# Kernel optimization log

Measured on AMD Instinct MI355X. Metric: run time of the kernel, lower is better.

Reference implementation:

```python
import jax, jax.numpy as jnp
import numpy as np

ALPHA = 0.1
BETA = 0.3
MARGIN = 2.0


def setup_inputs() -> dict:
    key = jax.random.key(0)
    k1, k2 = jax.random.split(key)
    prediction = jax.random.normal(k1, (8, 2048, 512), dtype=jnp.float32)
    target_seg = jax.random.randint(k2, (8, 2048), 0, 16, dtype=jnp.int64)
    return {"prediction": prediction, "target_seg": target_seg}


def _pairwise_sqdist(x):
    # x: [n, L, d] -> squared Euclidean distances [n, L, L] via a GEMM
    sq = jnp.sum(x * x, axis=-1)  # [n, L]
    inner = jnp.einsum('nld,nmd->nlm', x, x)  # [n, L, L]
    d2 = sq[:, :, None] + sq[:, None, :] - 2.0 * inner
    return jnp.maximum(d2, 0.0)


def _safe_sqrt(d2):
    # sqrt with zero (not NaN) gradient at 0, matching torch.cdist behavior
    pos = d2 > 0
    return jnp.where(pos, jnp.sqrt(jnp.where(pos, d2, 1.0)), 0.0)


def reference(prediction, target_seg):
    # y[i,j,k] = 1 if target_seg[i,j] == target_seg[i,k]
    y = (target_seg[:, :, None] == target_seg[:, None, :]).astype(prediction.dtype)
    d2 = _pairwise_sqdist(prediction)
    dist = _safe_sqrt(d2)
    hinge = jnp.maximum(MARGIN - dist, 0.0)
    loss = ALPHA * y * d2 + BETA * (1.0 - y) * hinge * hinge
    return jnp.mean(loss)
```

## Files before the change

### kernel.cpp

```cpp
#include <hip/hip_runtime.h>
#include <math.h>

#define L      2048
#define DDIM   512
#define NBATCH 8
#define BM     128
#define BN     128
#define BK     64
#define NKT    (DDIM / BK)
#define NTILE  (L / BM)
#define NPAIR  (NTILE * (NTILE + 1) / 2)
#define TOTAL_BLOCKS (NBATCH * NPAIR)

#define ALPHA  0.1f
#define BETA   0.3f
#define MARGIN 2.0f

typedef _Float16 f16x8 __attribute__((ext_vector_type(8)));
typedef __attribute__((ext_vector_type(16))) float f32x16;

#define TILE_SH 8192
#define BUFSZ   16384

#define GLOAD_LDS16(g, l) __builtin_amdgcn_global_load_lds(              \
    (const __attribute__((address_space(1))) unsigned int*)(g),          \
    (__attribute__((address_space(3))) unsigned int*)(l), 16, 0, 0)

__global__ __launch_bounds__(256) void conv_kernel(const float* __restrict__ pred,
                                                   _Float16* __restrict__ h,
                                                   float* __restrict__ sq) {
    int w     = threadIdx.x >> 6;
    int lane  = threadIdx.x & 63;
    int batch = blockIdx.x & 7;
    int idx   = blockIdx.x >> 3;
    int row   = batch * L + idx * 4 + w;
    const float* p = pred + (size_t)row * DDIM + lane * 8;
    float4 v0 = *(const float4*)(p);
    float4 v1 = *(const float4*)(p + 4);
    float vals[8] = {v0.x, v0.y, v0.z, v0.w, v1.x, v1.y, v1.z, v1.w};
    f16x8 hv;
    float s = 0.0f;
    #pragma unroll
    for (int i = 0; i < 8; ++i) {
        float x = vals[i];
        s = fmaf(x, x, s);
        hv[i] = (_Float16)x;
    }
    *(f16x8*)(h + (size_t)row * DDIM + lane * 8) = hv;
    #pragma unroll
    for (int off = 32; off > 0; off >>= 1) s += __shfl_down(s, off);
    if (lane == 0) sq[row] = s;
}

__global__ __launch_bounds__(256) void loss_kernel(
        const _Float16* __restrict__ h,
        const int*   __restrict__ seg,
        const float* __restrict__ sq,
        double*      __restrict__ partials) {
    __shared__ _Float16 smem[2 * BUFSZ];
    __shared__ double wred[4];

    int bid = blockIdx.x;
    int n = bid & 7;
    int p = bid >> 3;
    int tj = 0;
    while (true) {
        int rl2 = NTILE - tj;
        if (p < rl2) break;
        p -= rl2;
        ++tj;
    }
    int tk = tj + p;
    int j0 = tj * BM, k0 = tk * BN;

    int t    = threadIdx.x;
    int w    = t >> 6;
    int lane = t & 63;
    int wr   = w >> 1, wc = w & 1;
    int l31  = lane & 31;
    int hsel = lane >> 5;

    const _Float16* baseH = h + (size_t)n * L * DDIM;

    int rl8 = lane >> 3;
    int lc  = (lane & 7) ^ rl8;
    const _Float16* srcA = baseH + (size_t)(j0 + w * 32 + rl8) * DDIM + lc * 8;
    const _Float16* srcB = baseH + (size_t)(k0 + w * 32 + rl8) * DDIM + lc * 8;
    _Float16* dstA = smem + w * 2048;
    _Float16* dstB = smem + TILE_SH + w * 2048;

    #define STAGE(kt, cur)                                                    \
    {                                                                         \
        _Pragma("unroll")                                                     \
        for (int q = 0; q < 4; ++q) {                                         \
            GLOAD_LDS16(srcA + (size_t)(q * 8) * DDIM + (kt) * BK,            \
                        dstA + (cur) * BUFSZ + q * 512);                      \
            GLOAD_LDS16(srcB + (size_t)(q * 8) * DDIM + (kt) * BK,            \
                        dstB + (cur) * BUFSZ + q * 512);                      \
        }                                                                     \
    }

    int s7 = l31 & 7;
    int ra = (wr * 64 + l31) * 64;
    int rb = (wc * 64 + l31) * 64 + TILE_SH;
    int iA0 = ra + (((0 + hsel) ^ s7) << 3);
    int iA1 = ra + (((2 + hsel) ^ s7) << 3);
    int iA2 = ra + (((4 + hsel) ^ s7) << 3);
    int iA3 = ra + (((6 + hsel) ^ s7) << 3);
    int iB0 = rb + (((0 + hsel) ^ s7) << 3);
    int iB1 = rb + (((2 + hsel) ^ s7) << 3);
    int iB2 = rb + (((4 + hsel) ^ s7) << 3);
    int iB3 = rb + (((6 + hsel) ^ s7) << 3);

    f32x16 acc[2][2];
    #pragma unroll
    for (int m = 0; m < 2; ++m)
        #pragma unroll
        for (int nn = 0; nn < 2; ++nn)
            #pragma unroll
            for (int r = 0; r < 16; ++r) acc[m][nn][r] = 0.0f;

    STAGE(0, 0);
    asm volatile("s_waitcnt vmcnt(0)" ::: "memory");
    __builtin_amdgcn_s_barrier();

    #pragma unroll
    for (int kt = 0; kt < NKT; ++kt) {
        const int cur = kt & 1;
        if (kt + 1 < NKT) STAGE(kt + 1, cur ^ 1);

        #pragma unroll
        for (int ks = 0; ks < 4; ++ks) {
            int iA = (ks == 0) ? iA0 : (ks == 1) ? iA1 : (ks == 2) ? iA2 : iA3;
            int iB = (ks == 0) ? iB0 : (ks == 1) ? iB1 : (ks == 2) ? iB2 : iB3;
            f16x8 a0 = *(const f16x8*)&smem[iA + cur * BUFSZ];
            f16x8 a1 = *(const f16x8*)&smem[iA + cur * BUFSZ + 2048];
            f16x8 b0 = *(const f16x8*)&smem[iB + cur * BUFSZ];
            f16x8 b1 = *(const f16x8*)&smem[iB + cur * BUFSZ + 2048];
            acc[0][0] = __builtin_amdgcn_mfma_f32_32x32x16_f16(a0, b0, acc[0][0], 0, 0, 0);
            acc[0][1] = __builtin_amdgcn_mfma_f32_32x32x16_f16(a0, b1, acc[0][1], 0, 0, 0);
            acc[1][0] = __builtin_amdgcn_mfma_f32_32x32x16_f16(a1, b0, acc[1][0], 0, 0, 0);
            acc[1][1] = __builtin_amdgcn_mfma_f32_32x32x16_f16(a1, b1, acc[1][1], 0, 0, 0);
        }

        asm volatile("s_waitcnt vmcnt(0)" ::: "memory");
        __builtin_amdgcn_s_barrier();
    }

    const int*   segb = seg + n * L;
    const float* sqb  = sq + n * L;

    float lsum = 0.0f;
    #pragma unroll
    for (int nn = 0; nn < 2; ++nn) {
        int k = k0 + wc * 64 + nn * 32 + l31;
        float sqk = sqb[k];
        int   sgk = segb[k];
        #pragma unroll
        for (int m = 0; m < 2; ++m)
            #pragma unroll
            for (int r = 0; r < 16; ++r) {
                int j = j0 + wr * 64 + m * 32 + (r & 3) + 8 * (r >> 2) + 4 * hsel;
                float inner = acc[m][nn][r];
                float d2 = fmaxf(sqb[j] + sqk - 2.0f * inner, 0.0f);
                float v;
                if (segb[j] == sgk) {
                    v = ALPHA * d2;
                } else {
                    float dist = sqrtf(d2);
                    float hg = fmaxf(MARGIN - dist, 0.0f);
                    v = BETA * hg * hg;
                }
                lsum += v;
            }
    }

    double wgt = (tj == tk) ? 1.0 : 2.0;
    double dsum = (double)lsum * wgt;
    #pragma unroll
    for (int off = 32; off > 0; off >>= 1)
        dsum += __shfl_down(dsum, off);
    if (lane == 0) wred[w] = dsum;
    __syncthreads();
    if (t == 0) partials[bid] = (wred[0] + wred[1]) + (wred[2] + wred[3]);
}

__global__ __launch_bounds__(256) void reduce_kernel(const double* __restrict__ partials,
                                                     float* __restrict__ out,
                                                     int nPart, double invCount) {
    __shared__ double red[256];
    int t = threadIdx.x;
    double s = 0.0;
    for (int i = t; i < nPart; i += 256) s += partials[i];
    red[t] = s;
    __syncthreads();
    #pragma unroll
    for (int k = 128; k > 0; k >>= 1) {
        if (t < k) red[t] += red[t + k];
        __syncthreads();
    }
    if (t == 0) out[0] = (float)(red[0] * invCount);
}

extern "C" void kernel_launch(void* const* d_in, const int* in_sizes, int n_in,
                              void* d_out, int out_size, void* d_ws, size_t ws_size,
                              hipStream_t stream) {
    const float* pred = (const float*)d_in[0];
    const int*   seg  = (const int*)d_in[1];
    float* out = (float*)d_out;

    const size_t HALF = (size_t)NBATCH * L * DDIM;
    _Float16* h        = (_Float16*)d_ws;
    float*    sq       = (float*)(h + HALF);
    double*   partials = (double*)(sq + NBATCH * L);

    conv_kernel<<<NBATCH * L / 4, 256, 0, stream>>>(pred, h, sq);
    loss_kernel<<<TOTAL_BLOCKS, 256, 0, stream>>>(h, seg, sq, partials);
    reduce_kernel<<<1, 256, 0, stream>>>(partials, out, TOTAL_BLOCKS,
                                         1.0 / (double)((size_t)NBATCH * L * L));
}
```

Measured before the change: 62.59 us.

## Replace double-buffered K pipeline with single-buffered 128-wide K stages

```diff
diff --git a/kernel.cpp b/kernel.cpp
--- a/kernel.cpp
+++ b/kernel.cpp
@@ -6,8 +6,8 @@
 #define NBATCH 8
 #define BM     128
 #define BN     128
-#define BK     64
-#define NKT    (DDIM / BK)
+#define BK     128
+#define NST    (DDIM / BK)
 #define NTILE  (L / BM)
 #define NPAIR  (NTILE * (NTILE + 1) / 2)
 #define TOTAL_BLOCKS (NBATCH * NPAIR)
@@ -19,8 +19,8 @@
 typedef _Float16 f16x8 __attribute__((ext_vector_type(8)));
 typedef __attribute__((ext_vector_type(16))) float f32x16;
 
-#define TILE_SH 8192
-#define BUFSZ   16384
+#define AHALF  8192
+#define BOFF   16384
 
 #define GLOAD_LDS16(g, l) __builtin_amdgcn_global_load_lds(              \
     (const __attribute__((address_space(1))) unsigned int*)(g),          \
@@ -57,7 +57,7 @@
         const int*   __restrict__ seg,
         const float* __restrict__ sq,
         double*      __restrict__ partials) {
-    __shared__ _Float16 smem[2 * BUFSZ];
+    __shared__ _Float16 smem[32768];
     __shared__ double wred[4];
 
     int bid = blockIdx.x;
@@ -87,22 +87,24 @@
     const _Float16* srcA = baseH + (size_t)(j0 + w * 32 + rl8) * DDIM + lc * 8;
     const _Float16* srcB = baseH + (size_t)(k0 + w * 32 + rl8) * DDIM + lc * 8;
     _Float16* dstA = smem + w * 2048;
-    _Float16* dstB = smem + TILE_SH + w * 2048;
-
-    #define STAGE(kt, cur)                                                    \
+    _Float16* dstB = smem + BOFF + w * 2048;
+
+    #define STAGE(st)                                                         \
     {                                                                         \
         _Pragma("unroll")                                                     \
-        for (int q = 0; q < 4; ++q) {                                         \
-            GLOAD_LDS16(srcA + (size_t)(q * 8) * DDIM + (kt) * BK,            \
-                        dstA + (cur) * BUFSZ + q * 512);                      \
-            GLOAD_LDS16(srcB + (size_t)(q * 8) * DDIM + (kt) * BK,            \
-                        dstB + (cur) * BUFSZ + q * 512);                      \
-        }                                                                     \
+        for (int q = 0; q < 4; ++q)                                           \
+            _Pragma("unroll")                                                 \
+            for (int kh = 0; kh < 2; ++kh) {                                  \
+                GLOAD_LDS16(srcA + (size_t)(q * 8) * DDIM + (st) * BK + kh * 64, \
+                            dstA + kh * AHALF + q * 512);                     \
+                GLOAD_LDS16(srcB + (size_t)(q * 8) * DDIM + (st) * BK + kh * 64, \
+                            dstB + kh * AHALF + q * 512);                     \
+            }                                                                 \
     }
 
     int s7 = l31 & 7;
     int ra = (wr * 64 + l31) * 64;
-    int rb = (wc * 64 + l31) * 64 + TILE_SH;
+    int rb = (wc * 64 + l31) * 64 + BOFF;
     int iA0 = ra + (((0 + hsel) ^ s7) << 3);
     int iA1 = ra + (((2 + hsel) ^ s7) << 3);
     int iA2 = ra + (((4 + hsel) ^ s7) << 3);
@@ -120,31 +122,29 @@
             #pragma unroll
             for (int r = 0; r < 16; ++r) acc[m][nn][r] = 0.0f;
 
-    STAGE(0, 0);
-    asm volatile("s_waitcnt vmcnt(0)" ::: "memory");
-    __builtin_amdgcn_s_barrier();
-
-    #pragma unroll
-    for (int kt = 0; kt < NKT; ++kt) {
-        const int cur = kt & 1;
-        if (kt + 1 < NKT) STAGE(kt + 1, cur ^ 1);
+    #pragma unroll
+    for (int st = 0; st < NST; ++st) {
+        __syncthreads();
+        STAGE(st);
+        __syncthreads();
 
         #pragma unroll
-        for (int ks = 0; ks < 4; ++ks) {
-            int iA = (ks == 0) ? iA0 : (ks == 1) ? iA1 : (ks == 2) ? iA2 : iA3;
-            int iB = (ks == 0) ? iB0 : (ks == 1) ? iB1 : (ks == 2) ? iB2 : iB3;
-            f16x8 a0 = *(const f16x8*)&smem[iA + cur * BUFSZ];
-            f16x8 a1 = *(const f16x8*)&smem[iA + cur * BUFSZ + 2048];
-            f16x8 b0 = *(const f16x8*)&smem[iB + cur * BUFSZ];
-            f16x8 b1 = *(const f16x8*)&smem[iB + cur * BUFSZ + 2048];
+        for (int ks = 0; ks < 8; ++ks) {
+            int kq = ks & 3;
+            int kh = ks >> 2;
+            int iA = ((kq == 0) ? iA0 : (kq == 1) ? iA1 : (kq == 2) ? iA2 : iA3)
+                     + kh * AHALF;
+            int iB = ((kq == 0) ? iB0 : (kq == 1) ? iB1 : (kq == 2) ? iB2 : iB3)
+                     + kh * AHALF;
+            f16x8 a0 = *(const f16x8*)&smem[iA];
+            f16x8 a1 = *(const f16x8*)&smem[iA + 2048];
+            f16x8 b0 = *(const f16x8*)&smem[iB];
+            f16x8 b1 = *(const f16x8*)&smem[iB + 2048];
             acc[0][0] = __builtin_amdgcn_mfma_f32_32x32x16_f16(a0, b0, acc[0][0], 0, 0, 0);
             acc[0][1] = __builtin_amdgcn_mfma_f32_32x32x16_f16(a0, b1, acc[0][1], 0, 0, 0);
             acc[1][0] = __builtin_amdgcn_mfma_f32_32x32x16_f16(a1, b0, acc[1][0], 0, 0, 0);
             acc[1][1] = __builtin_amdgcn_mfma_f32_32x32x16_f16(a1, b1, acc[1][1], 0, 0, 0);
         }
-
-        asm volatile("s_waitcnt vmcnt(0)" ::: "memory");
-        __builtin_amdgcn_s_barrier();
     }
 
     const int*   segb = seg + n * L;
```

New measurement: 61.49 us. Within noise of the previous version (-1.8%).
